# Optimization experiments

Measured on AMD Instinct MI355X. Metric: run time of the kernel, lower is better.

Reference implementation:

```python
import jax, jax.numpy as jnp
import numpy as np

B, N, K = 2, 1024, 32
NUM_RBF = 16
NUM_POS = 16
EDGE_C = 128
MAXREL = 32
# atoms15 = [N, CA, C, O, virtual-CB, SC0..SC9]; 25 bb-bb pairs + 40 bb-sidechain pairs
_bb = np.arange(5)
SRC = np.concatenate([np.repeat(_bb, 5), np.repeat(np.arange(4), 10)])  # (65,)
DST = np.concatenate([np.tile(_bb, 5), np.tile(np.arange(5, 15), 4)])   # (65,)
P = 65
EDGE_IN = NUM_POS + NUM_RBF * P + 1  # 1057


def setup_inputs() -> dict:
    key = jax.random.key(0)
    ks = jax.random.split(key, 12)
    return {
        "atom14_coords": jax.random.normal(ks[0], (B, N, 14, 3), jnp.float32),
        "atom14_cond_mask": jnp.ones((B, N, 14), jnp.float32),
        "noise": jax.random.normal(ks[1], (B, N, 14, 3), jnp.float32),
        "residue_index": jnp.arange(B * N, dtype=jnp.int32).reshape(B, N),
        "asym_id": jax.random.randint(ks[2], (B, N), 0, 4, jnp.int32),
        "token_bonds": jax.random.uniform(ks[3], (B, N, N), jnp.float32),
        "is_ligand": jax.random.bernoulli(ks[4], 0.2, (B, N)),
        "pos_W": jax.random.normal(ks[5], (2 * MAXREL + 2, NUM_POS), jnp.float32) * 0.1,
        "pos_b": jax.random.normal(ks[6], (NUM_POS,), jnp.float32) * 0.1,
        "edge_W": jax.random.normal(ks[7], (EDGE_IN, EDGE_C), jnp.float32) * 0.02,
        "ln_gamma": jnp.ones((EDGE_C,), jnp.float32),
        "ln_beta": jnp.zeros((EDGE_C,), jnp.float32),
    }


def _gather_nodes(x, idx):
    # x: [B,N,...], idx: [B,N,K] -> [B,N,K,...]
    return jax.vmap(lambda a, i: a[i])(x, idx)


def _rbf(D):
    # D: [...,] -> [..., NUM_RBF]
    D_mu = jnp.linspace(2.0, 22.0, NUM_RBF)
    D_sigma = (22.0 - 2.0) / NUM_RBF
    return jnp.exp(-(((D[..., None] - D_mu) / D_sigma) ** 2))


def reference(atom14_coords, atom14_cond_mask, noise, residue_index, asym_id,
              token_bonds, is_ligand, pos_W, pos_b, edge_W, ln_gamma, ln_beta):
    X = atom14_coords + noise
    X = jnp.where(atom14_cond_mask[..., None] > 0, X, X[..., 1:2, :])
    CA = X[..., 1, :]                                  # [B,N,3]
    mask = atom14_cond_mask[..., 1]                    # [B,N]

    # --- KNN on CA distances ---
    mask_2D = mask[:, None, :] * mask[:, :, None]      # [B,N,N]
    dX = CA[:, None, :, :] - CA[:, :, None, :]
    D = mask_2D * jnp.sqrt(jnp.sum(dX * dX, -1) + 1e-6)
    D_max = jnp.max(D, -1, keepdims=True)
    D_adjust = D + (1.0 - mask_2D) * D_max
    neg_vals, E_idx = jax.lax.top_k(-D_adjust, K)      # smallest K, ascending
    D_neighbors = -neg_vals                            # [B,N,K]

    # --- virtual CB and 15-atom set ---
    b = X[:, :, 1, :] - X[:, :, 0, :]
    c = X[:, :, 2, :] - X[:, :, 1, :]
    a = jnp.cross(b, c)
    Cb = -0.58273431 * a + 0.56802827 * b - 0.54067466 * c + X[:, :, 1, :]
    atoms15 = jnp.concatenate([X[:, :, :4, :], Cb[:, :, None, :], X[:, :, 4:14, :]], axis=2)  # [B,N,15,3]

    # --- fused gather + pairwise distances + RBF over 65 atom pairs ---
    nb_atoms = _gather_nodes(atoms15, E_idx)           # [B,N,K,15,3]
    A = atoms15[:, :, SRC, :]                          # [B,N,65,3]
    Bn = nb_atoms[:, :, :, DST, :]                     # [B,N,K,65,3]
    diff = A[:, :, None, :, :] - Bn
    D_pairs = jnp.sqrt(jnp.sum(diff * diff, -1) + 1e-6)   # [B,N,K,65]
    RBF_all = _rbf(D_pairs).reshape(B, N, K, P * NUM_RBF)  # [B,N,K,1040]

    # --- positional encodings ---
    offset = residue_index[:, :, None] - residue_index[:, None, :]
    offset_nb = jnp.take_along_axis(offset, E_idx, axis=2)     # [B,N,K]
    chain_labels = asym_id  # use_multichain_encoding=True
    d_chains = (chain_labels[:, :, None] == chain_labels[:, None, :]).astype(jnp.int32)
    E_chains = jnp.take_along_axis(d_chains, E_idx, axis=2)    # [B,N,K]
    d = jnp.clip(offset_nb + MAXREL, 0, 2 * MAXREL) * E_chains + (1 - E_chains) * (2 * MAXREL + 1)
    d_onehot = jax.nn.one_hot(d, 2 * MAXREL + 2, dtype=jnp.float32)
    E_positional = d_onehot @ pos_W + pos_b                    # [B,N,K,16]

    # --- token bonds ---
    tb_mask = jnp.logical_or(is_ligand[:, :, None], is_ligand[:, None, :])
    tb = token_bonds * tb_mask.astype(token_bonds.dtype)
    tb_nb = jnp.take_along_axis(tb, E_idx, axis=2)[..., None]  # [B,N,K,1]

    # --- edge embedding + layernorm ---
    E = jnp.concatenate([E_positional, RBF_all, tb_nb], axis=-1)  # [B,N,K,1057]
    E = E @ edge_W                                                # [B,N,K,128]
    mu = jnp.mean(E, -1, keepdims=True)
    var = jnp.mean((E - mu) ** 2, -1, keepdims=True)
    E = (E - mu) / jnp.sqrt(var + 1e-5) * ln_gamma + ln_beta
    return (E, E_idx, D_neighbors)
```

## Files before the change

### kernel.cpp

```cpp
#include <hip/hip_runtime.h>
#include <math.h>

#define BB 2
#define NN 1024
#define KNN 32
#define PP 65
#define NRBF 16
#define EC 128
#define KPAD 1088
#define NCHUNK 17
#define NKT 34

typedef __attribute__((ext_vector_type(8))) short bf16x8;
typedef __attribute__((ext_vector_type(4))) float f32x4;

__device__ __forceinline__ ushort f2bf(float f) {
    union { float f; unsigned u; } v; v.f = f;
    unsigned r = v.u + 0x7fffu + ((v.u >> 16) & 1u);
    return (ushort)(r >> 16);
}

__global__ __launch_bounds__(256) void k_atoms(
    const float* __restrict__ coords, const float* __restrict__ mask,
    const float* __restrict__ noise, float* __restrict__ atoms15)
{
    int idx = blockIdx.x * blockDim.x + threadIdx.x;
    if (idx >= BB * NN) return;
    const float* c  = coords + (size_t)idx * 42;
    const float* nz = noise  + (size_t)idx * 42;
    const float* m  = mask   + (size_t)idx * 14;

    float X[14][3];
    float x1[3];
#pragma unroll
    for (int d = 0; d < 3; d++) x1[d] = c[3 + d] + nz[3 + d];
#pragma unroll
    for (int a = 0; a < 14; a++) {
        bool mm = m[a] > 0.0f;
#pragma unroll
        for (int d = 0; d < 3; d++) {
            float v = c[a * 3 + d] + nz[a * 3 + d];
            X[a][d] = mm ? v : x1[d];
        }
    }
    float bv[3], cv[3], av[3], cb[3];
#pragma unroll
    for (int d = 0; d < 3; d++) { bv[d] = X[1][d] - X[0][d]; cv[d] = X[2][d] - X[1][d]; }
    av[0] = bv[1] * cv[2] - bv[2] * cv[1];
    av[1] = bv[2] * cv[0] - bv[0] * cv[2];
    av[2] = bv[0] * cv[1] - bv[1] * cv[0];
#pragma unroll
    for (int d = 0; d < 3; d++)
        cb[d] = -0.58273431f * av[d] + 0.56802827f * bv[d] - 0.54067466f * cv[d] + X[1][d];

    float* o = atoms15 + (size_t)idx * 45;
#pragma unroll
    for (int a = 0; a < 4; a++)
#pragma unroll
        for (int d = 0; d < 3; d++) o[a * 3 + d] = X[a][d];
#pragma unroll
    for (int d = 0; d < 3; d++) o[4 * 3 + d] = cb[d];
#pragma unroll
    for (int a = 0; a < 10; a++)
#pragma unroll
        for (int d = 0; d < 3; d++) o[(5 + a) * 3 + d] = X[4 + a][d];
}

__global__ __launch_bounds__(256) void k_knn(
    const float* __restrict__ atoms15, const float* __restrict__ cond,
    float* __restrict__ out_idx_f, float* __restrict__ out_d, int* __restrict__ eidx)
{
    __shared__ float Dadj[NN];
    __shared__ float m2s[NN];
    __shared__ float redv[4];
    __shared__ int   redi[4];
    __shared__ float rmax[4];

    int row = blockIdx.x;
    int b = row >> 10, i = row & (NN - 1);
    int t = threadIdx.x;
    const float* ab = atoms15 + (size_t)b * NN * 45;
    float cax = ab[(size_t)i * 45 + 3];
    float cay = ab[(size_t)i * 45 + 4];
    float caz = ab[(size_t)i * 45 + 5];
    float mi = cond[(size_t)row * 14 + 1];

    float lmax = -1e30f;
    for (int j = t; j < NN; j += 256) {
        float dx = cax - ab[(size_t)j * 45 + 3];
        float dy = cay - ab[(size_t)j * 45 + 4];
        float dz = caz - ab[(size_t)j * 45 + 5];
        float mj = cond[((size_t)b * NN + j) * 14 + 1];
        float m2 = mi * mj;
        float D = m2 * sqrtf(dx * dx + dy * dy + dz * dz + 1e-6f);
        Dadj[j] = D; m2s[j] = m2;
        lmax = fmaxf(lmax, D);
    }
#pragma unroll
    for (int off = 32; off > 0; off >>= 1) lmax = fmaxf(lmax, __shfl_xor(lmax, off));
    int wv = t >> 6, ln = t & 63;
    if (ln == 0) rmax[wv] = lmax;
    __syncthreads();
    float Dmax = fmaxf(fmaxf(rmax[0], rmax[1]), fmaxf(rmax[2], rmax[3]));
    for (int j = t; j < NN; j += 256) Dadj[j] += (1.0f - m2s[j]) * Dmax;
    __syncthreads();

    for (int k = 0; k < KNN; k++) {
        float bvv = 1e30f; int bii = NN;
        for (int j = t; j < NN; j += 256) {
            float v = Dadj[j];
            if (v < bvv || (v == bvv && j < bii)) { bvv = v; bii = j; }
        }
#pragma unroll
        for (int off = 1; off < 64; off <<= 1) {
            float ov = __shfl_xor(bvv, off);
            int   oi = __shfl_xor(bii, off);
            if (ov < bvv || (ov == bvv && oi < bii)) { bvv = ov; bii = oi; }
        }
        if (ln == 0) { redv[wv] = bvv; redi[wv] = bii; }
        __syncthreads();
        if (t == 0) {
            float bv2 = redv[0]; int bi2 = redi[0];
            for (int w = 1; w < 4; w++) {
                if (redv[w] < bv2 || (redv[w] == bv2 && redi[w] < bi2)) { bv2 = redv[w]; bi2 = redi[w]; }
            }
            out_idx_f[(size_t)row * KNN + k] = (float)bi2;
            out_d  [(size_t)row * KNN + k] = bv2;
            eidx   [(size_t)row * KNN + k] = bi2;
            Dadj[bi2] = 1e30f;
        }
        __syncthreads();
    }
}

__global__ __launch_bounds__(256) void k_wprep(const float* __restrict__ W,
                                               ushort* __restrict__ wf)
{
    int x = blockIdx.x * 256 + threadIdx.x;
    if (x >= NKT * 8 * 64) return;
    int l = x & 63;
    int n16 = (x >> 6) & 7;
    int kt = x >> 9;
    int col = n16 * 16 + (l & 15);
    int kb  = kt * 32 + (l >> 4) * 8;
    ushort v[8];
#pragma unroll
    for (int j = 0; j < 8; j++) {
        int k = kb + j;
        float f = (k < 1057) ? W[(size_t)k * EC + col] : 0.0f;
        v[j] = f2bf(f);
    }
    *(uint4*)&wf[(size_t)x * 8] = *(uint4*)&v[0];
}

__global__ __launch_bounds__(256) void k_edge(
    const float* __restrict__ atoms15, const int* __restrict__ eidx,
    const int* __restrict__ resi, const int* __restrict__ asym,
    const float* __restrict__ tbonds, const int* __restrict__ islig,
    const float* __restrict__ posW, const float* __restrict__ posb,
    const ushort* __restrict__ wfrag, const float* __restrict__ gamma_,
    const float* __restrict__ beta_, float* __restrict__ outE)
{
    __shared__ int   nb[64];
    __shared__ float tbv[64];
    __shared__ float Crow[2][45];
    __shared__ float Brow[64][45];
    __shared__ float epos[64][16];
    __shared__ float Dp[64][PP];
    __shared__ __attribute__((aligned(16))) ushort F[64][72];
    __shared__ float part[2][64][2];

    int blk = blockIdx.x;
    int row0 = blk * 2;
    int b = row0 >> 10;
    int t = threadIdx.x;

    if (t < 64) nb[t] = eidx[(size_t)row0 * KNN + t];
    __syncthreads();

    if (t < 90) {
        int e = t / 45, r = t - e * 45;
        Crow[e][r] = atoms15[((size_t)(row0 + e)) * 45 + r];
    }
    {
        int e = t & 63;
        const float* src = atoms15 + ((size_t)(b * NN) + nb[e]) * 45;
#pragma unroll
        for (int q = 0; q < 12; q++) {
            int r = (t >> 6) * 12 + q;
            if (r < 45) Brow[e][r] = src[r];
        }
    }
    for (int x = t; x < 64 * 16; x += 256) {
        int e = x >> 4, r = x & 15;
        int ri = row0 + (e >> 5);
        int ii = ri & (NN - 1);
        int j = nb[e];
        int off = resi[(b << 10) + ii] - resi[(b << 10) + j];
        bool same = (asym[(b << 10) + ii] == asym[(b << 10) + j]);
        int d = same ? min(max(off + 32, 0), 64) : 65;
        epos[e][r] = posW[d * 16 + r] + posb[r];
    }
    if (t < 64) {
        int ri = row0 + (t >> 5);
        int ii = ri & (NN - 1);
        int j = nb[t];
        bool lg = (islig[(b << 10) + ii] != 0) || (islig[(b << 10) + j] != 0);
        tbv[t] = lg ? tbonds[((size_t)((b << 10) + ii)) * NN + j] : 0.0f;
    }
    __syncthreads();

    for (int x = t; x < 64 * PP; x += 256) {
        int e = x / PP, p = x - e * PP;
        int s, dd;
        if (p < 25) { s = p / 5; dd = p - s * 5; }
        else { int q = p - 25; s = q / 10; dd = 5 + (q - s * 10); }
        int cc = e >> 5;
        float dx = Crow[cc][s * 3 + 0] - Brow[e][dd * 3 + 0];
        float dy = Crow[cc][s * 3 + 1] - Brow[e][dd * 3 + 1];
        float dz = Crow[cc][s * 3 + 2] - Brow[e][dd * 3 + 2];
        Dp[e][p] = sqrtf(dx * dx + dy * dy + dz * dz + 1e-6f);
    }
    __syncthreads();

    const int l  = t & 63;
    const int w  = t >> 6;
    const int wm = w >> 1, wn = w & 1;
    const int lc = l & 15, g = l >> 4;

    f32x4 acc[2][4] = {};

    for (int c = 0; c < NCHUNK; c++) {
        {
            int e = l;
            int fb = w;
            float vals[16];
            if (c == 0 && fb == 0) {
#pragma unroll
                for (int i2 = 0; i2 < 16; i2++) vals[i2] = epos[e][i2];
            } else if (c == 16 && fb >= 2) {
#pragma unroll
                for (int i2 = 0; i2 < 16; i2++) vals[i2] = 0.0f;
                if (fb == 2) vals[0] = tbv[e];
            } else {
                int p = 4 * c + fb - 1;
                float d = Dp[e][p];
#pragma unroll
                for (int i2 = 0; i2 < 16; i2++) {
                    float u = (d - (2.0f + (float)i2 * (20.0f / 15.0f))) * 0.8f;
                    vals[i2] = __expf(-u * u);
                }
            }
            ushort us[16];
#pragma unroll
            for (int i2 = 0; i2 < 16; i2++) us[i2] = f2bf(vals[i2]);
            *(uint4*)&F[e][fb * 16]     = *(uint4*)&us[0];
            *(uint4*)&F[e][fb * 16 + 8] = *(uint4*)&us[8];
        }
        __syncthreads();

#pragma unroll
        for (int ks = 0; ks < 2; ks++) {
            bf16x8 a0 = *(const bf16x8*)&F[wm * 32 + lc][ks * 32 + 8 * g];
            bf16x8 a1 = *(const bf16x8*)&F[wm * 32 + 16 + lc][ks * 32 + 8 * g];
            int kt = c * 2 + ks;
#pragma unroll
            for (int ni = 0; ni < 4; ni++) {
                bf16x8 bfg = *(const bf16x8*)&wfrag[(((size_t)kt * 8 + wn * 4 + ni) * 64 + l) * 8];
                acc[0][ni] = __builtin_amdgcn_mfma_f32_16x16x32_bf16(a0, bfg, acc[0][ni], 0, 0, 0);
                acc[1][ni] = __builtin_amdgcn_mfma_f32_16x16x32_bf16(a1, bfg, acc[1][ni], 0, 0, 0);
            }
        }
        __syncthreads();
    }

    float gv[4], bev[4];
#pragma unroll
    for (int ni = 0; ni < 4; ni++) {
        int col = wn * 64 + ni * 16 + lc;
        gv[ni]  = gamma_[col];
        bev[ni] = beta_[col];
    }
#pragma unroll
    for (int mi = 0; mi < 2; mi++)
#pragma unroll
        for (int reg = 0; reg < 4; reg++) {
            float s = 0.0f, q = 0.0f;
#pragma unroll
            for (int ni = 0; ni < 4; ni++) {
                float v = acc[mi][ni][reg];
                s += v; q += v * v;
            }
#pragma unroll
            for (int m = 1; m < 16; m <<= 1) {
                s += __shfl_xor(s, m);
                q += __shfl_xor(q, m);
            }
            int srow = wm * 32 + mi * 16 + g * 4 + reg;
            if (lc == 0) { part[wn][srow][0] = s; part[wn][srow][1] = q; }
        }
    __syncthreads();
#pragma unroll
    for (int mi = 0; mi < 2; mi++)
#pragma unroll
        for (int reg = 0; reg < 4; reg++) {
            int srow = wm * 32 + mi * 16 + g * 4 + reg;
            float s = part[0][srow][0] + part[1][srow][0];
            float q = part[0][srow][1] + part[1][srow][1];
            float mu  = s * (1.0f / 128.0f);
            float var = q * (1.0f / 128.0f) - mu * mu;
            float rstd = rsqrtf(var + 1e-5f);
            size_t obase = ((size_t)blk * 64 + srow) * EC;
#pragma unroll
            for (int ni = 0; ni < 4; ni++) {
                float v = (acc[mi][ni][reg] - mu) * rstd * gv[ni] + bev[ni];
                outE[obase + wn * 64 + ni * 16 + lc] = v;
            }
        }
}

extern "C" void kernel_launch(void* const* d_in, const int* in_sizes, int n_in,
                              void* d_out, int out_size, void* d_ws, size_t ws_size,
                              hipStream_t stream)
{
    const float* coords = (const float*)d_in[0];
    const float* cond   = (const float*)d_in[1];
    const float* noise  = (const float*)d_in[2];
    const int*   resi   = (const int*)d_in[3];
    const int*   asym   = (const int*)d_in[4];
    const float* tbonds = (const float*)d_in[5];
    const int*   islig  = (const int*)d_in[6];
    const float* posW   = (const float*)d_in[7];
    const float* posb   = (const float*)d_in[8];
    const float* edgeW  = (const float*)d_in[9];
    const float* gamma_ = (const float*)d_in[10];
    const float* beta_  = (const float*)d_in[11];

    float* outE   = (float*)d_out;
    float* outIdx = outE + (size_t)BB * NN * KNN * EC;
    float* outD   = outIdx + (size_t)BB * NN * KNN;

    float*  atoms15 = (float*)d_ws;
    int*    eidx    = (int*)((char*)d_ws + 368640);
    ushort* wfrag   = (ushort*)((char*)d_ws + 368640 + 262144);

    k_wprep<<<(NKT * 8 * 64 + 255) / 256, 256, 0, stream>>>(edgeW, wfrag);
    k_atoms<<<(BB * NN + 255) / 256, 256, 0, stream>>>(coords, cond, noise, atoms15);
    k_knn<<<BB * NN, 256, 0, stream>>>(atoms15, cond, outIdx, outD, eidx);
    k_edge<<<BB * NN / 2, 256, 0, stream>>>(atoms15, eidx, resi, asym, tbonds, islig,
                                            posW, posb, wfrag, gamma_, beta_, outE);
}
```

Baseline: 245.6 us.

## Use per-wave register top-K in KNN and double-buffer edge feature tiles

The KNN kernel now keeps each thread's four distances in registers, has every wavefront pick its own 32 smallest using only shuffles, then merges the four 128-candidate lists in one wavefront. This removes the two block barriers and the single-thread serial reduction that ran on each of the 32 selection rounds. The edge kernel double-buffers the bf16 RBF feature tile, so the next chunk is computed while MFMAs consume the current one, which drops one barrier per chunk at the cost of more LDS.

```diff
diff --git a/kernel.cpp b/kernel.cpp
--- a/kernel.cpp
+++ b/kernel.cpp
@@ -72,13 +72,14 @@
 {
     __shared__ float Dadj[NN];
     __shared__ float m2s[NN];
-    __shared__ float redv[4];
-    __shared__ int   redi[4];
     __shared__ float rmax[4];
+    __shared__ float candv[128];
+    __shared__ int   candj[128];
 
     int row = blockIdx.x;
     int b = row >> 10, i = row & (NN - 1);
     int t = threadIdx.x;
+    int ln = t & 63, wv = t >> 6;
     const float* ab = atoms15 + (size_t)b * NN * 45;
     float cax = ab[(size_t)i * 45 + 3];
     float cay = ab[(size_t)i * 45 + 4];
@@ -98,38 +99,63 @@
     }
 #pragma unroll
     for (int off = 32; off > 0; off >>= 1) lmax = fmaxf(lmax, __shfl_xor(lmax, off));
-    int wv = t >> 6, ln = t & 63;
     if (ln == 0) rmax[wv] = lmax;
     __syncthreads();
     float Dmax = fmaxf(fmaxf(rmax[0], rmax[1]), fmaxf(rmax[2], rmax[3]));
     for (int j = t; j < NN; j += 256) Dadj[j] += (1.0f - m2s[j]) * Dmax;
     __syncthreads();
 
+    const int base = wv * 256 + ln;
+    float v0 = Dadj[base];
+    float v1 = Dadj[base + 64];
+    float v2 = Dadj[base + 128];
+    float v3 = Dadj[base + 192];
+
+    float selv = 0.0f; int seli = 0;
     for (int k = 0; k < KNN; k++) {
-        float bvv = 1e30f; int bii = NN;
-        for (int j = t; j < NN; j += 256) {
-            float v = Dadj[j];
-            if (v < bvv || (v == bvv && j < bii)) { bvv = v; bii = j; }
-        }
+        float bv = v0; int bj = base;
+        if (v1 < bv) { bv = v1; bj = base + 64;  }
+        if (v2 < bv) { bv = v2; bj = base + 128; }
+        if (v3 < bv) { bv = v3; bj = base + 192; }
 #pragma unroll
         for (int off = 1; off < 64; off <<= 1) {
-            float ov = __shfl_xor(bvv, off);
-            int   oi = __shfl_xor(bii, off);
-            if (ov < bvv || (ov == bvv && oi < bii)) { bvv = ov; bii = oi; }
-        }
-        if (ln == 0) { redv[wv] = bvv; redi[wv] = bii; }
-        __syncthreads();
-        if (t == 0) {
-            float bv2 = redv[0]; int bi2 = redi[0];
-            for (int w = 1; w < 4; w++) {
-                if (redv[w] < bv2 || (redv[w] == bv2 && redi[w] < bi2)) { bv2 = redv[w]; bi2 = redi[w]; }
-            }
-            out_idx_f[(size_t)row * KNN + k] = (float)bi2;
-            out_d  [(size_t)row * KNN + k] = bv2;
-            eidx   [(size_t)row * KNN + k] = bi2;
-            Dadj[bi2] = 1e30f;
-        }
-        __syncthreads();
+            float ov = __shfl_xor(bv, off);
+            int   oj = __shfl_xor(bj, off);
+            if (ov < bv || (ov == bv && oj < bj)) { bv = ov; bj = oj; }
+        }
+        if (ln == k) { selv = bv; seli = bj; }
+        if (bj == base)            v0 = 1e30f;
+        else if (bj == base + 64)  v1 = 1e30f;
+        else if (bj == base + 128) v2 = 1e30f;
+        else if (bj == base + 192) v3 = 1e30f;
+    }
+    if (ln < KNN) { candv[wv * KNN + ln] = selv; candj[wv * KNN + ln] = seli; }
+    __syncthreads();
+
+    if (wv == 0) {
+        float c0v = candv[ln];      int c0j = candj[ln];
+        float c1v = candv[64 + ln]; int c1j = candj[64 + ln];
+        float fv = 0.0f; int fj = 0;
+        for (int k = 0; k < KNN; k++) {
+            float bv; int bj;
+            if (c0v < c1v || (c0v == c1v && c0j < c1j)) { bv = c0v; bj = c0j; }
+            else                                        { bv = c1v; bj = c1j; }
+#pragma unroll
+            for (int off = 1; off < 64; off <<= 1) {
+                float ov = __shfl_xor(bv, off);
+                int   oj = __shfl_xor(bj, off);
+                if (ov < bv || (ov == bv && oj < bj)) { bv = ov; bj = oj; }
+            }
+            if (ln == k) { fv = bv; fj = bj; }
+            if (bj == c0j) c0v = 1e30f;
+            if (bj == c1j) c1v = 1e30f;
+        }
+        if (ln < KNN) {
+            size_t o = (size_t)row * KNN + ln;
+            out_d[o]     = fv;
+            out_idx_f[o] = (float)fj;
+            eidx[o]      = fj;
+        }
     }
 }
 
@@ -167,7 +193,7 @@
     __shared__ float Brow[64][45];
     __shared__ float epos[64][16];
     __shared__ float Dp[64][PP];
-    __shared__ __attribute__((aligned(16))) ushort F[64][72];
+    __shared__ __attribute__((aligned(16))) ushort F[2][64][72];
     __shared__ float part[2][64][2];
 
     int blk = blockIdx.x;
@@ -230,39 +256,44 @@
 
     f32x4 acc[2][4] = {};
 
+    auto STAGE = [&](int cs, int buf) {
+        int e = l;
+        int fb = w;
+        float vals[16];
+        if (cs == 0 && fb == 0) {
+#pragma unroll
+            for (int i2 = 0; i2 < 16; i2++) vals[i2] = epos[e][i2];
+        } else if (cs == 16 && fb >= 2) {
+#pragma unroll
+            for (int i2 = 0; i2 < 16; i2++) vals[i2] = 0.0f;
+            if (fb == 2) vals[0] = tbv[e];
+        } else {
+            int p = 4 * cs + fb - 1;
+            float d = Dp[e][p];
+#pragma unroll
+            for (int i2 = 0; i2 < 16; i2++) {
+                float u = (d - (2.0f + (float)i2 * (20.0f / 15.0f))) * 0.8f;
+                vals[i2] = __expf(-u * u);
+            }
+        }
+        ushort us[16];
+#pragma unroll
+        for (int i2 = 0; i2 < 16; i2++) us[i2] = f2bf(vals[i2]);
+        *(uint4*)&F[buf][e][fb * 16]     = *(uint4*)&us[0];
+        *(uint4*)&F[buf][e][fb * 16 + 8] = *(uint4*)&us[8];
+    };
+
+    STAGE(0, 0);
+    __syncthreads();
+
     for (int c = 0; c < NCHUNK; c++) {
-        {
-            int e = l;
-            int fb = w;
-            float vals[16];
-            if (c == 0 && fb == 0) {
-#pragma unroll
-                for (int i2 = 0; i2 < 16; i2++) vals[i2] = epos[e][i2];
-            } else if (c == 16 && fb >= 2) {
-#pragma unroll
-                for (int i2 = 0; i2 < 16; i2++) vals[i2] = 0.0f;
-                if (fb == 2) vals[0] = tbv[e];
-            } else {
-                int p = 4 * c + fb - 1;
-                float d = Dp[e][p];
-#pragma unroll
-                for (int i2 = 0; i2 < 16; i2++) {
-                    float u = (d - (2.0f + (float)i2 * (20.0f / 15.0f))) * 0.8f;
-                    vals[i2] = __expf(-u * u);
-                }
-            }
-            ushort us[16];
-#pragma unroll
-            for (int i2 = 0; i2 < 16; i2++) us[i2] = f2bf(vals[i2]);
-            *(uint4*)&F[e][fb * 16]     = *(uint4*)&us[0];
-            *(uint4*)&F[e][fb * 16 + 8] = *(uint4*)&us[8];
-        }
-        __syncthreads();
+        int cur = c & 1;
+        if (c + 1 < NCHUNK) STAGE(c + 1, cur ^ 1);
 
 #pragma unroll
         for (int ks = 0; ks < 2; ks++) {
-            bf16x8 a0 = *(const bf16x8*)&F[wm * 32 + lc][ks * 32 + 8 * g];
-            bf16x8 a1 = *(const bf16x8*)&F[wm * 32 + 16 + lc][ks * 32 + 8 * g];
+            bf16x8 a0 = *(const bf16x8*)&F[cur][wm * 32 + lc][ks * 32 + 8 * g];
+            bf16x8 a1 = *(const bf16x8*)&F[cur][wm * 32 + 16 + lc][ks * 32 + 8 * g];
             int kt = c * 2 + ks;
 #pragma unroll
             for (int ni = 0; ni < 4; ni++) {
```

New measurement: 233.8 us. -4.8%, faster.
